# Performance work log

Measured on AMD Instinct MI355X. Metric: run time of the kernel, lower is better.

## Reference

```python
import jax, jax.numpy as jnp
import numpy as np

B, H, E, D = 16384, 1024, 64, 128  # batch, hidden, nb_entities, wh_units==we_units


def setup_inputs() -> dict:
    key = jax.random.key(0)
    k0, k1, k2 = jax.random.split(key, 3)
    hidden_state = jax.random.normal(k0, (B, H), dtype=jnp.float32)
    # Wh: Dense(wh_units) acting on H -> D
    Wh_w = jax.random.normal(k1, (H, D), dtype=jnp.float32) * 0.02
    Wh_b = jnp.zeros((D,), dtype=jnp.float32)
    # We: nb_entities separate Dense(we_units), stacked into one [E, D, D] tensor
    We_w = jax.random.normal(k2, (E, D, D), dtype=jnp.float32) * 0.02
    We_b = jnp.zeros((E, D), dtype=jnp.float32)
    return {"hidden_state": hidden_state, "Wh_w": Wh_w, "Wh_b": Wh_b,
            "We_w": We_w, "We_b": We_b}


def reference(hidden_state, Wh_w, Wh_b, We_w, We_b):
    # reduced_dimentionality = Wh(hidden_state)            [B, D]
    r = hidden_state @ Wh_w + Wh_b
    # per-entity Dense loop + concat + transpose == one batched GEMM -> [B, E, D]
    logits = jnp.einsum('bk,ekd->bed', r, We_w) + We_b[None, :, :]
    outputs = jax.nn.softmax(logits, axis=-1)               # [B, E, D]
    # second pass: We[i] applied to outputs[:, i, :]       [B, E, D]
    vt = jnp.einsum('bek,ekd->bed', outputs, We_w) + We_b[None, :, :]
    # transpose to [B, D, E] then reduce_sum over E == sum over entity axis
    result = vt.sum(axis=1)                                 # [B, D]
    return (outputs, result)
```

## Files before the change

### kernel.cpp

```cpp
#include <hip/hip_runtime.h>
#include <hip/hip_bf16.h>

typedef __attribute__((ext_vector_type(8))) short short8;
typedef __attribute__((ext_vector_type(4))) float f32x4;
typedef __attribute__((ext_vector_type(4))) unsigned int uint4v;
typedef __attribute__((ext_vector_type(2))) unsigned int uint2v;

#define NB 16384
#define NH 1024
#define NE 64
#define ND 128
#define BR 32
#define GRP 4

static __device__ __forceinline__ unsigned short f2b(float x) {
  unsigned int u = __builtin_bit_cast(unsigned int, x);
  unsigned int r = (u + 0x7fffu + ((u >> 16) & 1u)) >> 16;
  return (unsigned short)r;
}
static __device__ __forceinline__ float b2f_lo(unsigned int u) {
  return __builtin_bit_cast(float, u << 16);
}
static __device__ __forceinline__ float b2f_hi(unsigned int u) {
  return __builtin_bit_cast(float, u & 0xffff0000u);
}

static __device__ __forceinline__ void bar_sync() {
  __builtin_amdgcn_sched_barrier(0);
  asm volatile("s_waitcnt lgkmcnt(0)" ::: "memory");
  __builtin_amdgcn_sched_barrier(0);
  __builtin_amdgcn_s_barrier();
  __builtin_amdgcn_sched_barrier(0);
}

static __device__ __forceinline__ int swz(int row, int col) {
  return (row << 7) + ((((col >> 3) ^ (row & 15)) << 3) | (col & 7));
}
static __device__ __forceinline__ int pswz(int row, int eg, int col) {
  return ((row * GRP + eg) << 7) + ((((col >> 3) ^ (row & 15)) << 3) | (col & 7));
}

__global__ __launch_bounds__(256, 1) void k0_prep(
    const float* __restrict__ Wh_w, const float* __restrict__ We_w,
    const float* __restrict__ We_b,
    unsigned short* __restrict__ WeT, unsigned short* __restrict__ WhT,
    float* __restrict__ bsum)
{
  __shared__ float tile[32][33];
  const int bid = blockIdx.x, t = threadIdx.x;
  const int i = t >> 5, j = t & 31;
  if (bid < 1024) {
    const int e = bid >> 4, tr = (bid >> 2) & 3, tc = bid & 3;
    const float* src = We_w + (size_t)e * 16384;
#pragma unroll
    for (int k = 0; k < 4; ++k)
      tile[i + 8 * k][j] = src[(size_t)(tr * 32 + i + 8 * k) * 128 + tc * 32 + j];
    __syncthreads();
    unsigned short* dst = WeT + (size_t)e * 16384;
#pragma unroll
    for (int k = 0; k < 4; ++k) {
      int row = i + 8 * k;
      dst[(size_t)(tc * 32 + row) * 128 + tr * 32 + j] = f2b(tile[j][row]);
    }
  } else if (bid < 1152) {
    const int tb = bid - 1024, tr = tb >> 2, tc = tb & 3;
#pragma unroll
    for (int k = 0; k < 4; ++k)
      tile[i + 8 * k][j] = Wh_w[(size_t)(tr * 32 + i + 8 * k) * 128 + tc * 32 + j];
    __syncthreads();
#pragma unroll
    for (int k = 0; k < 4; ++k) {
      int row = i + 8 * k;
      WhT[(size_t)(tc * 32 + row) * 1024 + tr * 32 + j] = f2b(tile[j][row]);
    }
  } else {
    if (t < 128) {
      float s = 0.f;
      for (int e = 0; e < 64; ++e) s += We_b[e * 128 + t];
      bsum[t] = s;
    }
  }
}

__global__ __launch_bounds__(256, 2) void k1_rgemm(
    const float* __restrict__ hidden, const unsigned short* __restrict__ WhT,
    const float* __restrict__ Wh_b, unsigned short* __restrict__ r_g)
{
  const int t = threadIdx.x;
  const int w = t >> 6, l = t & 63, c = l & 15, g = l >> 4;
  const int bg = w & 1, dh = w >> 1;
  const int b = blockIdx.x * 32 + 16 * bg + c;
  const float* hrow = hidden + (size_t)b * NH;
  f32x4 acc[4];
#pragma unroll
  for (int mf = 0; mf < 4; ++mf) acc[mf] = (f32x4){0.f, 0.f, 0.f, 0.f};
#pragma unroll 2
  for (int ks = 0; ks < 32; ++ks) {
    const int k0 = 8 * g + 32 * ks;
    f32x4 h0 = *(const f32x4*)(hrow + k0);
    f32x4 h1 = *(const f32x4*)(hrow + k0 + 4);
    short8 bf;
    bf[0] = (short)f2b(h0[0]); bf[1] = (short)f2b(h0[1]);
    bf[2] = (short)f2b(h0[2]); bf[3] = (short)f2b(h0[3]);
    bf[4] = (short)f2b(h1[0]); bf[5] = (short)f2b(h1[1]);
    bf[6] = (short)f2b(h1[2]); bf[7] = (short)f2b(h1[3]);
#pragma unroll
    for (int mf = 0; mf < 4; ++mf) {
      short8 af = *(const short8*)(WhT + (size_t)(64 * dh + 16 * mf + c) * NH + k0);
      acc[mf] = __builtin_amdgcn_mfma_f32_16x16x32_bf16(af, bf, acc[mf], 0, 0, 0);
    }
  }
#pragma unroll
  for (int mf = 0; mf < 4; ++mf) {
    const int d0 = 64 * dh + 16 * mf + 4 * g;
    f32x4 bias = *(const f32x4*)(Wh_b + d0);
    f32x4 v = acc[mf] + bias;
    unsigned int lo = (unsigned)f2b(v[0]) | ((unsigned)f2b(v[1]) << 16);
    unsigned int hi = (unsigned)f2b(v[2]) | ((unsigned)f2b(v[3]) << 16);
    uint2v pk = {lo, hi};
    *(uint2v*)(r_g + (size_t)b * ND + d0) = pk;
  }
}

struct SmemK2 {
  union {
    unsigned short Pst[BR * GRP * 128];
    float obuf[BR * 128];
  };
  unsigned short r_lds[BR * 128];
  float sms[4][BR];
};

static __device__ __forceinline__ void load_we_frags(
    short8 (&f)[2][4], f32x4 (&bias)[2],
    const unsigned short* __restrict__ WeT, const float* __restrict__ We_b,
    int e, int w, int c, int g)
{
  const unsigned short* base = WeT + (size_t)e * (ND * ND);
#pragma unroll
  for (int mf = 0; mf < 2; ++mf) {
    const unsigned short* rowp = base + (size_t)(16 * (2 * w + mf) + c) * ND + 8 * g;
#pragma unroll
    for (int ks = 0; ks < 4; ++ks)
      f[mf][ks] = *(const short8*)(rowp + 32 * ks);
    bias[mf] = *(const f32x4*)(We_b + e * ND + 32 * w + 16 * mf + 4 * g);
  }
}

static __device__ __forceinline__ void store_p_slice(
    const SmemK2& sm, float* __restrict__ outP,
    int brow0, int e_prev, int slice, int t)
{
#pragma unroll
  for (int it = 0; it < 4; ++it) {
    const int flat = it * 1024 + t * 4;
    const int row = flat >> 7;
    const int col = flat & 127;
    uint2v u = *(const uint2v*)(&sm.Pst[pswz(row, slice, col)]);
    f32x4 v;
    v[0] = b2f_lo(u[0]); v[1] = b2f_hi(u[0]);
    v[2] = b2f_lo(u[1]); v[3] = b2f_hi(u[1]);
    float* dst = outP + ((size_t)(brow0 + row) * NE + e_prev) * ND + col;
    __builtin_nontemporal_store(v, (f32x4*)dst);
  }
}

static __device__ __forceinline__ void entity_body(
    int i, int en, int e_prev, bool do_store,
    int brow0, int w, int c, int g, int t,
    short8 (&cur)[2][4], short8 (&nxt)[2][4],
    f32x4 (&bcur)[2], f32x4 (&bnxt)[2], f32x4 (&acc2)[2][2],
    const unsigned short* __restrict__ WeT, const float* __restrict__ We_b,
    float* __restrict__ outP, SmemK2& sm)
{
  const int eg = i & 3, pg = (i + 3) & 3;
  f32x4 acc1[2][2];
#pragma unroll
  for (int mf = 0; mf < 2; ++mf)
#pragma unroll
    for (int nf = 0; nf < 2; ++nf) acc1[mf][nf] = (f32x4){0.f, 0.f, 0.f, 0.f};
#pragma unroll
  for (int ks = 0; ks < 4; ++ks) {
    short8 b1[2];
#pragma unroll
    for (int nf = 0; nf < 2; ++nf)
      b1[nf] = *(const short8*)(&sm.r_lds[swz(16 * nf + c, 8 * g + 32 * ks)]);
#pragma unroll
    for (int mf = 0; mf < 2; ++mf)
#pragma unroll
      for (int nf = 0; nf < 2; ++nf)
        acc1[mf][nf] = __builtin_amdgcn_mfma_f32_16x16x32_bf16(
            cur[mf][ks], b1[nf], acc1[mf][nf], 0, 0, 0);
  }
  load_we_frags(nxt, bnxt, WeT, We_b, en, w, c, g);
  __builtin_amdgcn_sched_barrier(0);
  if (do_store) store_p_slice(sm, outP, brow0, e_prev, pg, t);

#pragma unroll
  for (int mf = 0; mf < 2; ++mf)
#pragma unroll
    for (int nf = 0; nf < 2; ++nf) acc1[mf][nf] += bcur[mf];
  float s[2] = {0.f, 0.f};
#pragma unroll
  for (int nf = 0; nf < 2; ++nf) {
#pragma unroll
    for (int mf = 0; mf < 2; ++mf)
#pragma unroll
      for (int r = 0; r < 4; ++r) {
        float p = __expf(acc1[mf][nf][r]);
        acc1[mf][nf][r] = p;
        s[nf] += p;
      }
    s[nf] += __shfl_xor(s[nf], 16);
    s[nf] += __shfl_xor(s[nf], 32);
  }
  if (g == 0) {
#pragma unroll
    for (int nf = 0; nf < 2; ++nf) sm.sms[w][16 * nf + c] = s[nf];
  }
  bar_sync();
  float inv[2];
#pragma unroll
  for (int nf = 0; nf < 2; ++nf) {
    int b = 16 * nf + c;
    inv[nf] = 1.f / (sm.sms[0][b] + sm.sms[1][b] + sm.sms[2][b] + sm.sms[3][b]);
  }
#pragma unroll
  for (int mf = 0; mf < 2; ++mf)
#pragma unroll
    for (int nf = 0; nf < 2; ++nf) {
      f32x4 p = acc1[mf][nf] * inv[nf];
      unsigned int lo = (unsigned)f2b(p[0]) | ((unsigned)f2b(p[1]) << 16);
      unsigned int hi = (unsigned)f2b(p[2]) | ((unsigned)f2b(p[3]) << 16);
      uint2v pk = {lo, hi};
      *(uint2v*)(&sm.Pst[pswz(16 * nf + c, eg, 32 * w + 16 * mf + 4 * g)]) = pk;
    }
  bar_sync();

#pragma unroll
  for (int ks = 0; ks < 4; ++ks) {
    short8 a2[2];
#pragma unroll
    for (int mf2 = 0; mf2 < 2; ++mf2)
      a2[mf2] = *(const short8*)(&sm.Pst[pswz(16 * mf2 + c, eg, 8 * g + 32 * ks)]);
#pragma unroll
    for (int mf2 = 0; mf2 < 2; ++mf2)
#pragma unroll
      for (int n = 0; n < 2; ++n)
        acc2[mf2][n] = __builtin_amdgcn_mfma_f32_16x16x32_bf16(
            a2[mf2], cur[n][ks], acc2[mf2][n], 0, 0, 0);
  }
}

__global__ __launch_bounds__(256, 2) void k2_main(
    const unsigned short* __restrict__ r_g, const unsigned short* __restrict__ WeT,
    const float* __restrict__ We_b, const float* __restrict__ bsum,
    float* __restrict__ outP, float* __restrict__ outR)
{
  __shared__ SmemK2 sm;
  const int t = threadIdx.x;
  const int w = t >> 6, l = t & 63, c = l & 15, g = l >> 4;
  const int lb = (blockIdx.x & 7) * 64 + (blockIdx.x >> 3);
  const int brow0 = lb * BR;
  const int e0 = (((lb >> 6) + lb) & 7) << 3;

  for (int i = t; i < BR * 16; i += 256) {
    int row = i >> 4, ch = i & 15;
    uint4v v = *(const uint4v*)(r_g + (size_t)(brow0 + row) * ND + ch * 8);
    *(uint4v*)(&sm.r_lds[swz(row, ch * 8)]) = v;
  }
  const float bs0 = bsum[32 * w + c];
  const float bs1 = bsum[32 * w + 16 + c];

  f32x4 acc2[2][2];
#pragma unroll
  for (int i = 0; i < 2; ++i)
#pragma unroll
    for (int j = 0; j < 2; ++j) acc2[i][j] = (f32x4){0.f, 0.f, 0.f, 0.f};

  short8 wa[2][4], wb[2][4];
  f32x4 ba[2], bb[2];
  load_we_frags(wa, ba, WeT, We_b, e0, w, c, g);
  bar_sync();

#pragma unroll 1
  for (int i = 0; i < NE; i += 2) {
    const int eB = (e0 + i + 1) & 63, eC = (e0 + i + 2) & 63;
    const int pA = (e0 + i + 63) & 63, pB = (e0 + i) & 63;
    entity_body(i,     eB, pA, i > 0, brow0, w, c, g, t,
                wa, wb, ba, bb, acc2, WeT, We_b, outP, sm);
    entity_body(i + 1, eC, pB, true,  brow0, w, c, g, t,
                wb, wa, bb, ba, acc2, WeT, We_b, outP, sm);
  }
  store_p_slice(sm, outP, brow0, (e0 + 63) & 63, 3, t);

  bar_sync();
#pragma unroll
  for (int mf2 = 0; mf2 < 2; ++mf2)
#pragma unroll
    for (int n = 0; n < 2; ++n) {
      float bs = n ? bs1 : bs0;
#pragma unroll
      for (int r = 0; r < 4; ++r)
        sm.obuf[(16 * mf2 + 4 * g + r) * ND + 32 * w + 16 * n + c] =
            acc2[mf2][n][r] + bs;
    }
  bar_sync();
  {
    const int orow = t >> 5, ocol = (t & 31) * 4;
#pragma unroll
    for (int it = 0; it < 4; ++it) {
      const int row = orow + 8 * it;
      f32x4 v = *(const f32x4*)(&sm.obuf[row * ND + ocol]);
      __builtin_nontemporal_store(
          v, (f32x4*)(outR + (size_t)(brow0 + row) * ND + ocol));
    }
  }
}

extern "C" void kernel_launch(void* const* d_in, const int* in_sizes, int n_in,
                              void* d_out, int out_size, void* d_ws, size_t ws_size,
                              hipStream_t stream)
{
  (void)in_sizes; (void)n_in; (void)out_size; (void)ws_size;
  const float* hidden = (const float*)d_in[0];
  const float* Wh_w   = (const float*)d_in[1];
  const float* Wh_b   = (const float*)d_in[2];
  const float* We_w   = (const float*)d_in[3];
  const float* We_b   = (const float*)d_in[4];
  float* outP = (float*)d_out;
  float* outR = outP + (size_t)NB * NE * ND;

  char* ws = (char*)d_ws;
  unsigned short* WeT = (unsigned short*)(ws);
  unsigned short* WhT = (unsigned short*)(ws + 2097152);
  unsigned short* r_g = (unsigned short*)(ws + 2097152 + 262144);
  float* bsum         = (float*)(ws + 2097152 + 262144 + 4194304);

  k0_prep<<<1153, 256, 0, stream>>>(Wh_w, We_w, We_b, WeT, WhT, bsum);
  k1_rgemm<<<512, 256, 0, stream>>>(hidden, WhT, Wh_b, r_g);
  k2_main<<<512, 256, 0, stream>>>(r_g, WeT, We_b, bsum, outP, outR);
}
```

Baseline: 223.0 us.

## Fuse Wh GEMM into main kernel and defer softmax normalization

```diff
diff --git a/kernel.cpp b/kernel.cpp
--- a/kernel.cpp
+++ b/kernel.cpp
@@ -11,7 +11,6 @@
 #define NE 64
 #define ND 128
 #define BR 32
-#define GRP 4
 
 static __device__ __forceinline__ unsigned short f2b(float x) {
   unsigned int u = __builtin_bit_cast(unsigned int, x);
@@ -35,9 +34,6 @@
 
 static __device__ __forceinline__ int swz(int row, int col) {
   return (row << 7) + ((((col >> 3) ^ (row & 15)) << 3) | (col & 7));
-}
-static __device__ __forceinline__ int pswz(int row, int eg, int col) {
-  return ((row * GRP + eg) << 7) + ((((col >> 3) ^ (row & 15)) << 3) | (col & 7));
 }
 
 __global__ __launch_bounds__(256, 1) void k0_prep(
@@ -82,53 +78,14 @@
   }
 }
 
-__global__ __launch_bounds__(256, 2) void k1_rgemm(
-    const float* __restrict__ hidden, const unsigned short* __restrict__ WhT,
-    const float* __restrict__ Wh_b, unsigned short* __restrict__ r_g)
-{
-  const int t = threadIdx.x;
-  const int w = t >> 6, l = t & 63, c = l & 15, g = l >> 4;
-  const int bg = w & 1, dh = w >> 1;
-  const int b = blockIdx.x * 32 + 16 * bg + c;
-  const float* hrow = hidden + (size_t)b * NH;
-  f32x4 acc[4];
-#pragma unroll
-  for (int mf = 0; mf < 4; ++mf) acc[mf] = (f32x4){0.f, 0.f, 0.f, 0.f};
-#pragma unroll 2
-  for (int ks = 0; ks < 32; ++ks) {
-    const int k0 = 8 * g + 32 * ks;
-    f32x4 h0 = *(const f32x4*)(hrow + k0);
-    f32x4 h1 = *(const f32x4*)(hrow + k0 + 4);
-    short8 bf;
-    bf[0] = (short)f2b(h0[0]); bf[1] = (short)f2b(h0[1]);
-    bf[2] = (short)f2b(h0[2]); bf[3] = (short)f2b(h0[3]);
-    bf[4] = (short)f2b(h1[0]); bf[5] = (short)f2b(h1[1]);
-    bf[6] = (short)f2b(h1[2]); bf[7] = (short)f2b(h1[3]);
-#pragma unroll
-    for (int mf = 0; mf < 4; ++mf) {
-      short8 af = *(const short8*)(WhT + (size_t)(64 * dh + 16 * mf + c) * NH + k0);
-      acc[mf] = __builtin_amdgcn_mfma_f32_16x16x32_bf16(af, bf, acc[mf], 0, 0, 0);
-    }
-  }
-#pragma unroll
-  for (int mf = 0; mf < 4; ++mf) {
-    const int d0 = 64 * dh + 16 * mf + 4 * g;
-    f32x4 bias = *(const f32x4*)(Wh_b + d0);
-    f32x4 v = acc[mf] + bias;
-    unsigned int lo = (unsigned)f2b(v[0]) | ((unsigned)f2b(v[1]) << 16);
-    unsigned int hi = (unsigned)f2b(v[2]) | ((unsigned)f2b(v[3]) << 16);
-    uint2v pk = {lo, hi};
-    *(uint2v*)(r_g + (size_t)b * ND + d0) = pk;
-  }
-}
-
 struct SmemK2 {
   union {
-    unsigned short Pst[BR * GRP * 128];
+    unsigned short Pst[2][BR * 128];
     float obuf[BR * 128];
   };
   unsigned short r_lds[BR * 128];
-  float sms[4][BR];
+  float sms[2][4][BR];
+  float invr[2][BR];
 };
 
 static __device__ __forceinline__ void load_we_frags(
@@ -149,31 +106,35 @@
 
 static __device__ __forceinline__ void store_p_slice(
     const SmemK2& sm, float* __restrict__ outP,
-    int brow0, int e_prev, int slice, int t)
+    int brow0, int e_prev, int sp, int t)
 {
 #pragma unroll
   for (int it = 0; it < 4; ++it) {
     const int flat = it * 1024 + t * 4;
     const int row = flat >> 7;
     const int col = flat & 127;
-    uint2v u = *(const uint2v*)(&sm.Pst[pswz(row, slice, col)]);
+    const float inv = sm.invr[sp][row];
+    uint2v u = *(const uint2v*)(&sm.Pst[sp][swz(row, col)]);
     f32x4 v;
-    v[0] = b2f_lo(u[0]); v[1] = b2f_hi(u[0]);
-    v[2] = b2f_lo(u[1]); v[3] = b2f_hi(u[1]);
+    v[0] = b2f_lo(u[0]) * inv; v[1] = b2f_hi(u[0]) * inv;
+    v[2] = b2f_lo(u[1]) * inv; v[3] = b2f_hi(u[1]) * inv;
     float* dst = outP + ((size_t)(brow0 + row) * NE + e_prev) * ND + col;
     __builtin_nontemporal_store(v, (f32x4*)dst);
   }
 }
 
 static __device__ __forceinline__ void entity_body(
-    int i, int en, int e_prev, bool do_store,
-    int brow0, int w, int c, int g, int t,
+    int i, int en, int ep, int brow0, int w, int c, int g, int t,
     short8 (&cur)[2][4], short8 (&nxt)[2][4],
     f32x4 (&bcur)[2], f32x4 (&bnxt)[2], f32x4 (&acc2)[2][2],
     const unsigned short* __restrict__ WeT, const float* __restrict__ We_b,
     float* __restrict__ outP, SmemK2& sm)
 {
-  const int eg = i & 3, pg = (i + 3) & 3;
+  const int si = i & 1, sp = si ^ 1;
+  load_we_frags(nxt, bnxt, WeT, We_b, en, w, c, g);
+  __builtin_amdgcn_sched_barrier(0);
+  if (i > 0) store_p_slice(sm, outP, brow0, ep, sp, t);
+  __builtin_amdgcn_sched_barrier(0);
   f32x4 acc1[2][2];
 #pragma unroll
   for (int mf = 0; mf < 2; ++mf)
@@ -192,10 +153,6 @@
         acc1[mf][nf] = __builtin_amdgcn_mfma_f32_16x16x32_bf16(
             cur[mf][ks], b1[nf], acc1[mf][nf], 0, 0, 0);
   }
-  load_we_frags(nxt, bnxt, WeT, We_b, en, w, c, g);
-  __builtin_amdgcn_sched_barrier(0);
-  if (do_store) store_p_slice(sm, outP, brow0, e_prev, pg, t);
-
 #pragma unroll
   for (int mf = 0; mf < 2; ++mf)
 #pragma unroll
@@ -215,45 +172,68 @@
     s[nf] += __shfl_xor(s[nf], 32);
   }
   if (g == 0) {
-#pragma unroll
-    for (int nf = 0; nf < 2; ++nf) sm.sms[w][16 * nf + c] = s[nf];
-  }
-  bar_sync();
-  float inv[2];
-#pragma unroll
-  for (int nf = 0; nf < 2; ++nf) {
-    int b = 16 * nf + c;
-    inv[nf] = 1.f / (sm.sms[0][b] + sm.sms[1][b] + sm.sms[2][b] + sm.sms[3][b]);
+    sm.sms[si][w][c] = s[0];
+    sm.sms[si][w][16 + c] = s[1];
   }
 #pragma unroll
   for (int mf = 0; mf < 2; ++mf)
 #pragma unroll
     for (int nf = 0; nf < 2; ++nf) {
-      f32x4 p = acc1[mf][nf] * inv[nf];
+      f32x4 p = acc1[mf][nf];
       unsigned int lo = (unsigned)f2b(p[0]) | ((unsigned)f2b(p[1]) << 16);
       unsigned int hi = (unsigned)f2b(p[2]) | ((unsigned)f2b(p[3]) << 16);
       uint2v pk = {lo, hi};
-      *(uint2v*)(&sm.Pst[pswz(16 * nf + c, eg, 32 * w + 16 * mf + 4 * g)]) = pk;
+      *(uint2v*)(&sm.Pst[si][swz(16 * nf + c, 32 * w + 16 * mf + 4 * g)]) = pk;
     }
   bar_sync();
-
-#pragma unroll
-  for (int ks = 0; ks < 4; ++ks) {
+  f32x4 inv4[2];
+#pragma unroll
+  for (int mf2 = 0; mf2 < 2; ++mf2) {
+    const int b0 = 16 * mf2 + 4 * g;
+    f32x4 sv = *(const f32x4*)(&sm.sms[si][0][b0]);
+    sv += *(const f32x4*)(&sm.sms[si][1][b0]);
+    sv += *(const f32x4*)(&sm.sms[si][2][b0]);
+    sv += *(const f32x4*)(&sm.sms[si][3][b0]);
+#pragma unroll
+    for (int r = 0; r < 4; ++r) inv4[mf2][r] = __builtin_amdgcn_rcpf(sv[r]);
+  }
+  if (g == 0) {
+#pragma unroll
+    for (int nf = 0; nf < 2; ++nf) {
+      const int b = 16 * nf + c;
+      float st = sm.sms[si][0][b] + sm.sms[si][1][b] +
+                 sm.sms[si][2][b] + sm.sms[si][3][b];
+      sm.invr[si][b] = __builtin_amdgcn_rcpf(st);
+    }
+  }
+  f32x4 eacc[2][2];
+#pragma unroll
+  for (int mf2 = 0; mf2 < 2; ++mf2)
+#pragma unroll
+    for (int n = 0; n < 2; ++n) eacc[mf2][n] = (f32x4){0.f, 0.f, 0.f, 0.f};
+#pragma unroll
+  for (int ks2 = 0; ks2 < 4; ++ks2) {
     short8 a2[2];
 #pragma unroll
     for (int mf2 = 0; mf2 < 2; ++mf2)
-      a2[mf2] = *(const short8*)(&sm.Pst[pswz(16 * mf2 + c, eg, 8 * g + 32 * ks)]);
+      a2[mf2] = *(const short8*)(&sm.Pst[si][swz(16 * mf2 + c, 8 * g + 32 * ks2)]);
 #pragma unroll
     for (int mf2 = 0; mf2 < 2; ++mf2)
 #pragma unroll
       for (int n = 0; n < 2; ++n)
-        acc2[mf2][n] = __builtin_amdgcn_mfma_f32_16x16x32_bf16(
-            a2[mf2], cur[n][ks], acc2[mf2][n], 0, 0, 0);
-  }
+        eacc[mf2][n] = __builtin_amdgcn_mfma_f32_16x16x32_bf16(
+            a2[mf2], cur[n][ks2], eacc[mf2][n], 0, 0, 0);
+  }
+#pragma unroll
+  for (int mf2 = 0; mf2 < 2; ++mf2)
+#pragma unroll
+    for (int n = 0; n < 2; ++n)
+      acc2[mf2][n] += eacc[mf2][n] * inv4[mf2];
 }
 
 __global__ __launch_bounds__(256, 2) void k2_main(
-    const unsigned short* __restrict__ r_g, const unsigned short* __restrict__ WeT,
+    const float* __restrict__ hidden, const unsigned short* __restrict__ WhT,
+    const float* __restrict__ Wh_b, const unsigned short* __restrict__ WeT,
     const float* __restrict__ We_b, const float* __restrict__ bsum,
     float* __restrict__ outP, float* __restrict__ outR)
 {
@@ -264,35 +244,77 @@
   const int brow0 = lb * BR;
   const int e0 = (((lb >> 6) + lb) & 7) << 3;
 
-  for (int i = t; i < BR * 16; i += 256) {
-    int row = i >> 4, ch = i & 15;
-    uint4v v = *(const uint4v*)(r_g + (size_t)(brow0 + row) * ND + ch * 8);
-    *(uint4v*)(&sm.r_lds[swz(row, ch * 8)]) = v;
-  }
-  const float bs0 = bsum[32 * w + c];
-  const float bs1 = bsum[32 * w + 16 + c];
-
-  f32x4 acc2[2][2];
-#pragma unroll
-  for (int i = 0; i < 2; ++i)
-#pragma unroll
-    for (int j = 0; j < 2; ++j) acc2[i][j] = (f32x4){0.f, 0.f, 0.f, 0.f};
-
   short8 wa[2][4], wb[2][4];
   f32x4 ba[2], bb[2];
   load_we_frags(wa, ba, WeT, We_b, e0, w, c, g);
+
+  {
+    f32x4 pacc[2][2];
+#pragma unroll
+    for (int mf = 0; mf < 2; ++mf)
+#pragma unroll
+      for (int nf = 0; nf < 2; ++nf) pacc[mf][nf] = (f32x4){0.f, 0.f, 0.f, 0.f};
+    const float* h0p = hidden + (size_t)(brow0 + c) * NH;
+    const float* h1p = hidden + (size_t)(brow0 + 16 + c) * NH;
+    const unsigned short* wa0 = WhT + (size_t)(32 * w + c) * NH;
+    const unsigned short* wa1 = WhT + (size_t)(32 * w + 16 + c) * NH;
+#pragma unroll 2
+    for (int ks = 0; ks < 32; ++ks) {
+      const int k0 = 8 * g + 32 * ks;
+      f32x4 ha = *(const f32x4*)(h0p + k0);
+      f32x4 hb = *(const f32x4*)(h0p + k0 + 4);
+      f32x4 hc = *(const f32x4*)(h1p + k0);
+      f32x4 hd = *(const f32x4*)(h1p + k0 + 4);
+      short8 bf0, bf1;
+      bf0[0] = (short)f2b(ha[0]); bf0[1] = (short)f2b(ha[1]);
+      bf0[2] = (short)f2b(ha[2]); bf0[3] = (short)f2b(ha[3]);
+      bf0[4] = (short)f2b(hb[0]); bf0[5] = (short)f2b(hb[1]);
+      bf0[6] = (short)f2b(hb[2]); bf0[7] = (short)f2b(hb[3]);
+      bf1[0] = (short)f2b(hc[0]); bf1[1] = (short)f2b(hc[1]);
+      bf1[2] = (short)f2b(hc[2]); bf1[3] = (short)f2b(hc[3]);
+      bf1[4] = (short)f2b(hd[0]); bf1[5] = (short)f2b(hd[1]);
+      bf1[6] = (short)f2b(hd[2]); bf1[7] = (short)f2b(hd[3]);
+      short8 af0 = *(const short8*)(wa0 + k0);
+      short8 af1 = *(const short8*)(wa1 + k0);
+      pacc[0][0] = __builtin_amdgcn_mfma_f32_16x16x32_bf16(af0, bf0, pacc[0][0], 0, 0, 0);
+      pacc[0][1] = __builtin_amdgcn_mfma_f32_16x16x32_bf16(af0, bf1, pacc[0][1], 0, 0, 0);
+      pacc[1][0] = __builtin_amdgcn_mfma_f32_16x16x32_bf16(af1, bf0, pacc[1][0], 0, 0, 0);
+      pacc[1][1] = __builtin_amdgcn_mfma_f32_16x16x32_bf16(af1, bf1, pacc[1][1], 0, 0, 0);
+    }
+#pragma unroll
+    for (int mf = 0; mf < 2; ++mf) {
+      const int d0 = 32 * w + 16 * mf + 4 * g;
+      f32x4 bias = *(const f32x4*)(Wh_b + d0);
+#pragma unroll
+      for (int nf = 0; nf < 2; ++nf) {
+        f32x4 v = pacc[mf][nf] + bias;
+        unsigned int lo = (unsigned)f2b(v[0]) | ((unsigned)f2b(v[1]) << 16);
+        unsigned int hi = (unsigned)f2b(v[2]) | ((unsigned)f2b(v[3]) << 16);
+        uint2v pk = {lo, hi};
+        *(uint2v*)(&sm.r_lds[swz(16 * nf + c, d0)]) = pk;
+      }
+    }
+  }
+  const float bs0 = bsum[32 * w + c];
+  const float bs1 = bsum[32 * w + 16 + c];
   bar_sync();
+
+  f32x4 acc2[2][2];
+#pragma unroll
+  for (int i = 0; i < 2; ++i)
+#pragma unroll
+    for (int j = 0; j < 2; ++j) acc2[i][j] = (f32x4){0.f, 0.f, 0.f, 0.f};
 
 #pragma unroll 1
   for (int i = 0; i < NE; i += 2) {
     const int eB = (e0 + i + 1) & 63, eC = (e0 + i + 2) & 63;
     const int pA = (e0 + i + 63) & 63, pB = (e0 + i) & 63;
-    entity_body(i,     eB, pA, i > 0, brow0, w, c, g, t,
+    entity_body(i,     eB, pA, brow0, w, c, g, t,
                 wa, wb, ba, bb, acc2, WeT, We_b, outP, sm);
-    entity_body(i + 1, eC, pB, true,  brow0, w, c, g, t,
+    entity_body(i + 1, eC, pB, brow0, w, c, g, t,
                 wb, wa, bb, ba, acc2, WeT, We_b, outP, sm);
   }
-  store_p_slice(sm, outP, brow0, (e0 + 63) & 63, 3, t);
+  store_p_slice(sm, outP, brow0, (e0 + 63) & 63, 1, t);
 
   bar_sync();
 #pragma unroll
@@ -334,10 +356,8 @@
   char* ws = (char*)d_ws;
   unsigned short* WeT = (unsigned short*)(ws);
   unsigned short* WhT = (unsigned short*)(ws + 2097152);
-  unsigned short* r_g = (unsigned short*)(ws + 2097152 + 262144);
-  float* bsum         = (float*)(ws + 2097152 + 262144 + 4194304);
+  float* bsum         = (float*)(ws + 2097152 + 262144);
 
   k0_prep<<<1153, 256, 0, stream>>>(Wh_w, We_w, We_b, WeT, WhT, bsum);
-  k1_rgemm<<<512, 256, 0, stream>>>(hidden, WhT, Wh_b, r_g);
-  k2_main<<<512, 256, 0, stream>>>(r_g, WeT, We_b, bsum, outP, outR);
-}
+  k2_main<<<512, 256, 0, stream>>>(hidden, WhT, Wh_b, WeT, We_b, bsum, outP, outR);
+}
```

Result: slower. 247.4 us (+10.9%).

## Batch softmax output stores into 4-entity contiguous row segments with 8-slot LDS ring

Applied to the files above, without the earlier changes.

```diff
diff --git a/kernel.cpp b/kernel.cpp
--- a/kernel.cpp
+++ b/kernel.cpp
@@ -11,7 +11,6 @@
 #define NE 64
 #define ND 128
 #define BR 32
-#define GRP 4
 
 static __device__ __forceinline__ unsigned short f2b(float x) {
   unsigned int u = __builtin_bit_cast(unsigned int, x);
@@ -35,9 +34,6 @@
 
 static __device__ __forceinline__ int swz(int row, int col) {
   return (row << 7) + ((((col >> 3) ^ (row & 15)) << 3) | (col & 7));
-}
-static __device__ __forceinline__ int pswz(int row, int eg, int col) {
-  return ((row * GRP + eg) << 7) + ((((col >> 3) ^ (row & 15)) << 3) | (col & 7));
 }
 
 __global__ __launch_bounds__(256, 1) void k0_prep(
@@ -124,7 +120,7 @@
 
 struct SmemK2 {
   union {
-    unsigned short Pst[BR * GRP * 128];
+    unsigned short Pst[8][BR * 128];
     float obuf[BR * 128];
   };
   unsigned short r_lds[BR * 128];
@@ -147,33 +143,44 @@
   }
 }
 
-static __device__ __forceinline__ void store_p_slice(
+static __device__ __forceinline__ void store_group_part(
     const SmemK2& sm, float* __restrict__ outP,
-    int brow0, int e_prev, int slice, int t)
-{
-#pragma unroll
-  for (int it = 0; it < 4; ++it) {
-    const int flat = it * 1024 + t * 4;
-    const int row = flat >> 7;
-    const int col = flat & 127;
-    uint2v u = *(const uint2v*)(&sm.Pst[pswz(row, slice, col)]);
-    f32x4 v;
-    v[0] = b2f_lo(u[0]); v[1] = b2f_hi(u[0]);
-    v[2] = b2f_lo(u[1]); v[3] = b2f_hi(u[1]);
-    float* dst = outP + ((size_t)(brow0 + row) * NE + e_prev) * ND + col;
-    __builtin_nontemporal_store(v, (f32x4*)dst);
+    int brow0, int ebase4, int slot0, int part, int t)
+{
+  const int w = t >> 6, l = t & 63;
+#pragma unroll
+  for (int rr = 0; rr < 2; ++rr) {
+    const int row = 8 * part + 2 * w + rr;
+    float* dst = outP + ((size_t)(brow0 + row) * NE + ebase4) * ND;
+#pragma unroll
+    for (int it = 0; it < 2; ++it) {
+      const int f = it * 256 + l * 4;
+      const int k = f >> 7;
+      const int col = f & 127;
+      uint2v u = *(const uint2v*)(&sm.Pst[(slot0 + k) & 7][swz(row, col)]);
+      f32x4 v;
+      v[0] = b2f_lo(u[0]); v[1] = b2f_hi(u[0]);
+      v[2] = b2f_lo(u[1]); v[3] = b2f_hi(u[1]);
+      __builtin_nontemporal_store(v, (f32x4*)(dst + f));
+    }
   }
 }
 
 static __device__ __forceinline__ void entity_body(
-    int i, int en, int e_prev, bool do_store,
-    int brow0, int w, int c, int g, int t,
+    int i, int en, int e0, int brow0, int w, int c, int g, int t,
     short8 (&cur)[2][4], short8 (&nxt)[2][4],
     f32x4 (&bcur)[2], f32x4 (&bnxt)[2], f32x4 (&acc2)[2][2],
     const unsigned short* __restrict__ WeT, const float* __restrict__ We_b,
     float* __restrict__ outP, SmemK2& sm)
 {
-  const int eg = i & 3, pg = (i + 3) & 3;
+  const int si = i & 7;
+  load_we_frags(nxt, bnxt, WeT, We_b, en, w, c, g);
+  __builtin_amdgcn_sched_barrier(0);
+  if (i >= 4) {
+    const int gp = (i >> 2) - 1;
+    store_group_part(sm, outP, brow0, (e0 + 4 * gp) & 63, (4 * gp) & 7, i & 3, t);
+  }
+  __builtin_amdgcn_sched_barrier(0);
   f32x4 acc1[2][2];
 #pragma unroll
   for (int mf = 0; mf < 2; ++mf)
@@ -192,10 +199,6 @@
         acc1[mf][nf] = __builtin_amdgcn_mfma_f32_16x16x32_bf16(
             cur[mf][ks], b1[nf], acc1[mf][nf], 0, 0, 0);
   }
-  load_we_frags(nxt, bnxt, WeT, We_b, en, w, c, g);
-  __builtin_amdgcn_sched_barrier(0);
-  if (do_store) store_p_slice(sm, outP, brow0, e_prev, pg, t);
-
 #pragma unroll
   for (int mf = 0; mf < 2; ++mf)
 #pragma unroll
@@ -233,22 +236,21 @@
       unsigned int lo = (unsigned)f2b(p[0]) | ((unsigned)f2b(p[1]) << 16);
       unsigned int hi = (unsigned)f2b(p[2]) | ((unsigned)f2b(p[3]) << 16);
       uint2v pk = {lo, hi};
-      *(uint2v*)(&sm.Pst[pswz(16 * nf + c, eg, 32 * w + 16 * mf + 4 * g)]) = pk;
-    }
-  bar_sync();
-
-#pragma unroll
-  for (int ks = 0; ks < 4; ++ks) {
+      *(uint2v*)(&sm.Pst[si][swz(16 * nf + c, 32 * w + 16 * mf + 4 * g)]) = pk;
+    }
+  bar_sync();
+#pragma unroll
+  for (int ks2 = 0; ks2 < 4; ++ks2) {
     short8 a2[2];
 #pragma unroll
     for (int mf2 = 0; mf2 < 2; ++mf2)
-      a2[mf2] = *(const short8*)(&sm.Pst[pswz(16 * mf2 + c, eg, 8 * g + 32 * ks)]);
+      a2[mf2] = *(const short8*)(&sm.Pst[si][swz(16 * mf2 + c, 8 * g + 32 * ks2)]);
 #pragma unroll
     for (int mf2 = 0; mf2 < 2; ++mf2)
 #pragma unroll
       for (int n = 0; n < 2; ++n)
         acc2[mf2][n] = __builtin_amdgcn_mfma_f32_16x16x32_bf16(
-            a2[mf2], cur[n][ks], acc2[mf2][n], 0, 0, 0);
+            a2[mf2], cur[n][ks2], acc2[mf2][n], 0, 0, 0);
   }
 }
 
@@ -286,13 +288,14 @@
 #pragma unroll 1
   for (int i = 0; i < NE; i += 2) {
     const int eB = (e0 + i + 1) & 63, eC = (e0 + i + 2) & 63;
-    const int pA = (e0 + i + 63) & 63, pB = (e0 + i) & 63;
-    entity_body(i,     eB, pA, i > 0, brow0, w, c, g, t,
+    entity_body(i,     eB, e0, brow0, w, c, g, t,
                 wa, wb, ba, bb, acc2, WeT, We_b, outP, sm);
-    entity_body(i + 1, eC, pB, true,  brow0, w, c, g, t,
+    entity_body(i + 1, eC, e0, brow0, w, c, g, t,
                 wb, wa, bb, ba, acc2, WeT, We_b, outP, sm);
   }
-  store_p_slice(sm, outP, brow0, (e0 + 63) & 63, 3, t);
+#pragma unroll
+  for (int part = 0; part < 4; ++part)
+    store_group_part(sm, outP, brow0, (e0 + 60) & 63, 4, part, t);
 
   bar_sync();
 #pragma unroll
```

After: 237.4 us. 6.4% more time.

## Process entities in pairs to halve barriers per entity in fused softmax kernel

Applied to the files above, without the earlier changes.

```diff
diff --git a/kernel.cpp b/kernel.cpp
--- a/kernel.cpp
+++ b/kernel.cpp
@@ -11,7 +11,6 @@
 #define NE 64
 #define ND 128
 #define BR 32
-#define GRP 4
 
 static __device__ __forceinline__ unsigned short f2b(float x) {
   unsigned int u = __builtin_bit_cast(unsigned int, x);
@@ -35,9 +34,6 @@
 
 static __device__ __forceinline__ int swz(int row, int col) {
   return (row << 7) + ((((col >> 3) ^ (row & 15)) << 3) | (col & 7));
-}
-static __device__ __forceinline__ int pswz(int row, int eg, int col) {
-  return ((row * GRP + eg) << 7) + ((((col >> 3) ^ (row & 15)) << 3) | (col & 7));
 }
 
 __global__ __launch_bounds__(256, 1) void k0_prep(
@@ -124,11 +120,11 @@
 
 struct SmemK2 {
   union {
-    unsigned short Pst[BR * GRP * 128];
+    unsigned short Pst[4][BR * 128];
     float obuf[BR * 128];
   };
   unsigned short r_lds[BR * 128];
-  float sms[4][BR];
+  float sms[2][4][BR];
 };
 
 static __device__ __forceinline__ void load_we_frags(
@@ -156,7 +152,7 @@
     const int flat = it * 1024 + t * 4;
     const int row = flat >> 7;
     const int col = flat & 127;
-    uint2v u = *(const uint2v*)(&sm.Pst[pswz(row, slice, col)]);
+    uint2v u = *(const uint2v*)(&sm.Pst[slice][swz(row, col)]);
     f32x4 v;
     v[0] = b2f_lo(u[0]); v[1] = b2f_hi(u[0]);
     v[2] = b2f_lo(u[1]); v[3] = b2f_hi(u[1]);
@@ -165,20 +161,25 @@
   }
 }
 
-static __device__ __forceinline__ void entity_body(
-    int i, int en, int e_prev, bool do_store,
+static __device__ __forceinline__ void pair_body(
+    int i, int enA, int enB, int epA, int epB, bool do_store,
     int brow0, int w, int c, int g, int t,
-    short8 (&cur)[2][4], short8 (&nxt)[2][4],
-    f32x4 (&bcur)[2], f32x4 (&bnxt)[2], f32x4 (&acc2)[2][2],
+    short8 (&cur)[2][2][4], short8 (&nxt)[2][2][4],
+    f32x4 (&bcur)[2][2], f32x4 (&bnxt)[2][2], f32x4 (&acc2)[2][2],
     const unsigned short* __restrict__ WeT, const float* __restrict__ We_b,
     float* __restrict__ outP, SmemK2& sm)
 {
-  const int eg = i & 3, pg = (i + 3) & 3;
-  f32x4 acc1[2][2];
-#pragma unroll
-  for (int mf = 0; mf < 2; ++mf)
-#pragma unroll
-    for (int nf = 0; nf < 2; ++nf) acc1[mf][nf] = (f32x4){0.f, 0.f, 0.f, 0.f};
+  const int s0 = (2 * i) & 3, s1 = (2 * i + 1) & 3;
+  load_we_frags(nxt[0], bnxt[0], WeT, We_b, enA, w, c, g);
+  load_we_frags(nxt[1], bnxt[1], WeT, We_b, enB, w, c, g);
+  __builtin_amdgcn_sched_barrier(0);
+  f32x4 acc1[2][2][2];
+#pragma unroll
+  for (int en = 0; en < 2; ++en)
+#pragma unroll
+    for (int mf = 0; mf < 2; ++mf)
+#pragma unroll
+      for (int nf = 0; nf < 2; ++nf) acc1[en][mf][nf] = (f32x4){0.f, 0.f, 0.f, 0.f};
 #pragma unroll
   for (int ks = 0; ks < 4; ++ks) {
     short8 b1[2];
@@ -186,69 +187,87 @@
     for (int nf = 0; nf < 2; ++nf)
       b1[nf] = *(const short8*)(&sm.r_lds[swz(16 * nf + c, 8 * g + 32 * ks)]);
 #pragma unroll
+    for (int en = 0; en < 2; ++en)
+#pragma unroll
+      for (int mf = 0; mf < 2; ++mf)
+#pragma unroll
+        for (int nf = 0; nf < 2; ++nf)
+          acc1[en][mf][nf] = __builtin_amdgcn_mfma_f32_16x16x32_bf16(
+              cur[en][mf][ks], b1[nf], acc1[en][mf][nf], 0, 0, 0);
+  }
+  float s2[2][2];
+#pragma unroll
+  for (int en = 0; en < 2; ++en) {
+#pragma unroll
     for (int mf = 0; mf < 2; ++mf)
 #pragma unroll
-      for (int nf = 0; nf < 2; ++nf)
-        acc1[mf][nf] = __builtin_amdgcn_mfma_f32_16x16x32_bf16(
-            cur[mf][ks], b1[nf], acc1[mf][nf], 0, 0, 0);
-  }
-  load_we_frags(nxt, bnxt, WeT, We_b, en, w, c, g);
-  __builtin_amdgcn_sched_barrier(0);
-  if (do_store) store_p_slice(sm, outP, brow0, e_prev, pg, t);
-
-#pragma unroll
-  for (int mf = 0; mf < 2; ++mf)
-#pragma unroll
-    for (int nf = 0; nf < 2; ++nf) acc1[mf][nf] += bcur[mf];
-  float s[2] = {0.f, 0.f};
-#pragma unroll
-  for (int nf = 0; nf < 2; ++nf) {
+      for (int nf = 0; nf < 2; ++nf) acc1[en][mf][nf] += bcur[en][mf];
+#pragma unroll
+    for (int nf = 0; nf < 2; ++nf) {
+      float s = 0.f;
+#pragma unroll
+      for (int mf = 0; mf < 2; ++mf)
+#pragma unroll
+        for (int r = 0; r < 4; ++r) {
+          float p = __expf(acc1[en][mf][nf][r]);
+          acc1[en][mf][nf][r] = p;
+          s += p;
+        }
+      s += __shfl_xor(s, 16);
+      s += __shfl_xor(s, 32);
+      s2[en][nf] = s;
+    }
+  }
+  if (g == 0) {
+#pragma unroll
+    for (int en = 0; en < 2; ++en)
+#pragma unroll
+      for (int nf = 0; nf < 2; ++nf) sm.sms[en][w][16 * nf + c] = s2[en][nf];
+  }
+  __builtin_amdgcn_sched_barrier(0);
+  if (do_store) {
+    store_p_slice(sm, outP, brow0, epA, s0 ^ 2, t);
+    store_p_slice(sm, outP, brow0, epB, s1 ^ 2, t);
+  }
+  bar_sync();
+#pragma unroll
+  for (int en = 0; en < 2; ++en) {
+    float inv[2];
+#pragma unroll
+    for (int nf = 0; nf < 2; ++nf) {
+      const int b = 16 * nf + c;
+      inv[nf] = 1.f / (sm.sms[en][0][b] + sm.sms[en][1][b] +
+                       sm.sms[en][2][b] + sm.sms[en][3][b]);
+    }
+    const int slot = en ? s1 : s0;
 #pragma unroll
     for (int mf = 0; mf < 2; ++mf)
 #pragma unroll
-      for (int r = 0; r < 4; ++r) {
-        float p = __expf(acc1[mf][nf][r]);
-        acc1[mf][nf][r] = p;
-        s[nf] += p;
+      for (int nf = 0; nf < 2; ++nf) {
+        f32x4 p = acc1[en][mf][nf] * inv[nf];
+        unsigned int lo = (unsigned)f2b(p[0]) | ((unsigned)f2b(p[1]) << 16);
+        unsigned int hi = (unsigned)f2b(p[2]) | ((unsigned)f2b(p[3]) << 16);
+        uint2v pk = {lo, hi};
+        *(uint2v*)(&sm.Pst[slot][swz(16 * nf + c, 32 * w + 16 * mf + 4 * g)]) = pk;
       }
-    s[nf] += __shfl_xor(s[nf], 16);
-    s[nf] += __shfl_xor(s[nf], 32);
-  }
-  if (g == 0) {
-#pragma unroll
-    for (int nf = 0; nf < 2; ++nf) sm.sms[w][16 * nf + c] = s[nf];
-  }
-  bar_sync();
-  float inv[2];
-#pragma unroll
-  for (int nf = 0; nf < 2; ++nf) {
-    int b = 16 * nf + c;
-    inv[nf] = 1.f / (sm.sms[0][b] + sm.sms[1][b] + sm.sms[2][b] + sm.sms[3][b]);
-  }
-#pragma unroll
-  for (int mf = 0; mf < 2; ++mf)
-#pragma unroll
-    for (int nf = 0; nf < 2; ++nf) {
-      f32x4 p = acc1[mf][nf] * inv[nf];
-      unsigned int lo = (unsigned)f2b(p[0]) | ((unsigned)f2b(p[1]) << 16);
-      unsigned int hi = (unsigned)f2b(p[2]) | ((unsigned)f2b(p[3]) << 16);
-      uint2v pk = {lo, hi};
-      *(uint2v*)(&sm.Pst[pswz(16 * nf + c, eg, 32 * w + 16 * mf + 4 * g)]) = pk;
-    }
-  bar_sync();
-
-#pragma unroll
-  for (int ks = 0; ks < 4; ++ks) {
-    short8 a2[2];
-#pragma unroll
-    for (int mf2 = 0; mf2 < 2; ++mf2)
-      a2[mf2] = *(const short8*)(&sm.Pst[pswz(16 * mf2 + c, eg, 8 * g + 32 * ks)]);
-#pragma unroll
-    for (int mf2 = 0; mf2 < 2; ++mf2)
-#pragma unroll
-      for (int n = 0; n < 2; ++n)
-        acc2[mf2][n] = __builtin_amdgcn_mfma_f32_16x16x32_bf16(
-            a2[mf2], cur[n][ks], acc2[mf2][n], 0, 0, 0);
+  }
+  bar_sync();
+#pragma unroll
+  for (int en = 0; en < 2; ++en) {
+    const int slot = en ? s1 : s0;
+#pragma unroll
+    for (int ks2 = 0; ks2 < 4; ++ks2) {
+      short8 a2[2];
+#pragma unroll
+      for (int mf2 = 0; mf2 < 2; ++mf2)
+        a2[mf2] = *(const short8*)(&sm.Pst[slot][swz(16 * mf2 + c, 8 * g + 32 * ks2)]);
+#pragma unroll
+      for (int mf2 = 0; mf2 < 2; ++mf2)
+#pragma unroll
+        for (int n = 0; n < 2; ++n)
+          acc2[mf2][n] = __builtin_amdgcn_mfma_f32_16x16x32_bf16(
+              a2[mf2], cur[en][n][ks2], acc2[mf2][n], 0, 0, 0);
+    }
   }
 }
 
@@ -278,21 +297,23 @@
 #pragma unroll
     for (int j = 0; j < 2; ++j) acc2[i][j] = (f32x4){0.f, 0.f, 0.f, 0.f};
 
-  short8 wa[2][4], wb[2][4];
-  f32x4 ba[2], bb[2];
-  load_we_frags(wa, ba, WeT, We_b, e0, w, c, g);
-  bar_sync();
-
+  short8 wa[2][2][4], wb[2][2][4];
+  f32x4 ba[2][2], bb[2][2];
+  load_we_frags(wa[0], ba[0], WeT, We_b, e0, w, c, g);
+  load_we_frags(wa[1], ba[1], WeT, We_b, (e0 + 1) & 63, w, c, g);
+  bar_sync();
+
+#define E(x) ((e0 + (x)) & 63)
 #pragma unroll 1
-  for (int i = 0; i < NE; i += 2) {
-    const int eB = (e0 + i + 1) & 63, eC = (e0 + i + 2) & 63;
-    const int pA = (e0 + i + 63) & 63, pB = (e0 + i) & 63;
-    entity_body(i,     eB, pA, i > 0, brow0, w, c, g, t,
-                wa, wb, ba, bb, acc2, WeT, We_b, outP, sm);
-    entity_body(i + 1, eC, pB, true,  brow0, w, c, g, t,
-                wb, wa, bb, ba, acc2, WeT, We_b, outP, sm);
-  }
-  store_p_slice(sm, outP, brow0, (e0 + 63) & 63, 3, t);
+  for (int i = 0; i < 32; i += 2) {
+    pair_body(i,     E(2 * i + 2), E(2 * i + 3), E(2 * i - 2 + 64), E(2 * i - 1 + 64),
+              i > 0, brow0, w, c, g, t, wa, wb, ba, bb, acc2, WeT, We_b, outP, sm);
+    pair_body(i + 1, E(2 * i + 4), E(2 * i + 5), E(2 * i),          E(2 * i + 1),
+              true,  brow0, w, c, g, t, wb, wa, bb, ba, acc2, WeT, We_b, outP, sm);
+  }
+  store_p_slice(sm, outP, brow0, E(62), 2, t);
+  store_p_slice(sm, outP, brow0, E(63), 3, t);
+#undef E
 
   bar_sync();
 #pragma unroll
```

Result: slower. 250.6 us (+12.4%).
